# Kernel optimization log

Hardware: AMD Instinct MI355X
Metric: run time of the kernel (lower is better)

## Reference

```python
import jax, jax.numpy as jnp
import numpy as np

B, NELEC, D, NION = 2048, 32, 512, 8
NSPIN = 2
N = NELEC // NSPIN  # electrons per spin = orbital-matrix size = 16


def setup_inputs() -> dict:
    key = jax.random.key(0)
    ks = jax.random.split(key, 6)
    eq_inputs = jax.random.normal(ks[0], (B, NELEC, D), jnp.float32)
    r_ei = jax.random.normal(ks[1], (B, NELEC, NION, 3), jnp.float32)
    # learned params (stacked over the 2 spins; equal split so shapes match)
    W_lin = jax.random.normal(ks[2], (NSPIN, 2 * D, N), jnp.float32) * (0.5 / np.sqrt(D))
    b_lin = jax.random.normal(ks[3], (NSPIN, N), jnp.float32) * 0.1
    A_env = jax.random.normal(ks[4], (NSPIN, 3, 3, NION, N), jnp.float32) * 0.3
    w_ion = jax.random.normal(ks[5], (NSPIN, NION, N), jnp.float32)
    return dict(eq_inputs=eq_inputs, r_ei=r_ei, W_lin=W_lin, b_lin=b_lin,
                A_env=A_env, w_ion=w_ion)


def reference(eq_inputs, r_ei, W_lin, b_lin, A_env, w_ion):
    """Per-particle determinant antiequivariance layer.

    For each spin s and particle p, a doubly-equivariant orbital matrix
    M_p[j, k] = (y_p . W1[:,k] + y_j . W2[:,k] + b[k]) * env[j, k]
    is built (pair-concat dense split into two einsums to avoid the (B,n,n,2d)
    intermediate), with anisotropic exponential envelopes
    env[j, k] = sum_I w_ion[I,k] * exp(-||A[:,:,I,k] @ r_ei[j,I,:]||).
    Output per spin: y_p * det(M_p), stacked over spins -> (B, 2, n, d).
    """
    b, nelec, d = eq_inputs.shape
    n = nelec // NSPIN
    x = eq_inputs.reshape(b, NSPIN, n, d)            # spin_split=2 equal split
    r = r_ei.reshape(b, NSPIN, n, r_ei.shape[-2], 3)
    W1, W2 = W_lin[:, :d], W_lin[:, d:]
    # linear (doubly equivariant) part: (B, S, n_p, n_j, n_k)
    lin_p = jnp.einsum('bspf,sfk->bspk', x, W1)
    lin_j = jnp.einsum('bsjf,sfk->bsjk', x, W2) + b_lin[None, :, None, :]
    lin = lin_p[:, :, :, None, :] + lin_j[:, :, None, :, :]
    # anisotropic exponential envelopes: exp(-||A (r - R)||), combined over ions
    ar = jnp.einsum('bsjip,spqik->bsjiqk', r, A_env)        # (B,S,n,I,3,k)
    env = jnp.exp(-jnp.sqrt(jnp.sum(ar * ar, axis=-2)))     # (B,S,n,I,k)
    env = jnp.einsum('bsjik,sik->bsjk', env, w_ion)         # (B,S,n_j,n_k)
    M = lin * env[:, :, None, :, :]                         # (B,S,n_p,n_j,n_k)
    dets = jnp.linalg.det(M)                                # (B,S,n_p)
    # y_p * det(M_p), per spin (stacked over the spin axis)
    return x * dets[..., None]                              # (B,S,n,d)
```

## Files before the change

kernel.cpp:

```cpp
#include <hip/hip_runtime.h>
#include <cstdint>
#include <cstddef>

#define NSPIN 2
#define NPART 16
#define DDIM  512
#define NION  8
#define NB    2

#define RS_OFF     0
#define GRAM_OFF   768
#define LINP_OFF   (GRAM_OFF + 1152)
#define LINJ_OFF   (LINP_OFF + 320)
#define ENV_OFF    (LINJ_OFF + 320)
#define DETS_OFF   (ENV_OFF + 320)
#define LDS_FLOATS (DETS_OFF + 16)
#define LDS_BYTES  (LDS_FLOATS * 4)

#define WS_GRAM_F  16384

typedef short bf16x8 __attribute__((ext_vector_type(8)));
typedef float f32x4  __attribute__((ext_vector_type(4)));

__device__ __forceinline__ short bfc(float x) {
    unsigned u = __float_as_uint(x);
    u += 0x7FFFu + ((u >> 16) & 1u);
    return (short)(u >> 16);
}

#define DPPMAXU(k, ctrl) { unsigned o_ = (unsigned)__builtin_amdgcn_update_dpp(0, (int)(k), (ctrl), 0xF, 0xF, true); (k) = (k) > o_ ? (k) : o_; }

__global__ void __launch_bounds__(256)
prep_kernel(const float* __restrict__ WL, const float* __restrict__ AE,
            const float* __restrict__ WI, float* __restrict__ WSF)
{
    const int t = threadIdx.x;
    if (blockIdx.x < 16) {
        int slot = blockIdx.x * 256 + t;
        int spin = slot >> 11;
        int rem  = slot & 2047;
        int half = rem >> 10;
        int ks   = (rem >> 6) & 15;
        int lane = rem & 63;
        int cc2  = lane & 15, hh = lane >> 4;
        const float* src = WL + (size_t)spin * (2 * DDIM * NPART)
                         + ((size_t)(half * 512 + ks * 32 + hh * 8)) * NPART + cc2;
        ushort u[8];
        #pragma unroll
        for (int e = 0; e < 8; ++e) u[e] = (ushort)bfc(src[e * NPART]);
        uint4 pk;
        pk.x = (unsigned)u[0] | ((unsigned)u[1] << 16);
        pk.y = (unsigned)u[2] | ((unsigned)u[3] << 16);
        pk.z = (unsigned)u[4] | ((unsigned)u[5] << 16);
        pk.w = (unsigned)u[6] | ((unsigned)u[7] << 16);
        ((uint4*)WSF)[slot] = pk;
    } else {
        int s  = t >> 7;
        int ke = (t >> 3) & 15;
        int i  = t & 7;
        const float* Ag = AE + (size_t)s * (9 * NION * NPART);
        float a00 = Ag[((0 * 3 + 0) * NION + i) * NPART + ke];
        float a01 = Ag[((0 * 3 + 1) * NION + i) * NPART + ke];
        float a02 = Ag[((0 * 3 + 2) * NION + i) * NPART + ke];
        float a10 = Ag[((1 * 3 + 0) * NION + i) * NPART + ke];
        float a11 = Ag[((1 * 3 + 1) * NION + i) * NPART + ke];
        float a12 = Ag[((1 * 3 + 2) * NION + i) * NPART + ke];
        float a20 = Ag[((2 * 3 + 0) * NION + i) * NPART + ke];
        float a21 = Ag[((2 * 3 + 1) * NION + i) * NPART + ke];
        float a22 = Ag[((2 * 3 + 2) * NION + i) * NPART + ke];
        float* g = WSF + WS_GRAM_F + t * 8;
        g[0] = a00 * a00 + a01 * a01 + a02 * a02;
        g[1] = a10 * a10 + a11 * a11 + a12 * a12;
        g[2] = a20 * a20 + a21 * a21 + a22 * a22;
        g[3] = a00 * a10 + a01 * a11 + a02 * a12;
        g[4] = a00 * a20 + a01 * a21 + a02 * a22;
        g[5] = a10 * a20 + a11 * a21 + a12 * a22;
        g[6] = WI[(size_t)s * (NION * NPART) + i * NPART + ke];
        g[7] = 0.f;
    }
}

__global__ void __launch_bounds__(128, 4)
ppdet_kernel(const float* __restrict__ EQ, const float* __restrict__ RE,
             const float* __restrict__ WSF, const float* __restrict__ BL,
             float* __restrict__ OUT)
{
    extern __shared__ float ls[];
    const int t  = threadIdx.x;
    const int s  = blockIdx.x >> 10;
    const int b0 = (blockIdx.x & 1023) * NB;

    const int l  = t & 63;
    const int w  = t >> 6;
    const int c  = l & 15;
    const int h4 = l >> 4;
    const int jr = t & 15;

    #pragma unroll
    for (int it = 0; it < 6; ++it) {
        int idx = it * 128 + t;
        int ibuf = idx / 384, rem = idx % 384;
        int e = rem >> 4, j = rem & 15;
        ls[RS_OFF + idx] = RE[((size_t)(b0 + ibuf) * 32 + s * 16 + j) * 24 + e];
    }
    #pragma unroll
    for (int it = 0; it < 8; ++it) {
        int idx = it * 128 + t;
        int ke = idx >> 6, rem = idx & 63;
        ls[GRAM_OFF + ke * 72 + rem] = WSF[WS_GRAM_F + s * 1024 + idx];
    }
    const float blv = BL[s * NPART + c];
    __syncthreads();

    for (int ib = 0; ib < NB; ++ib) {
        const int b = b0 + ib;

        {
            const float* xg = EQ + ((size_t)(b * 32 + s * 16 + c)) * DDIM + h4 * 8;
            const uint4* wb = (const uint4*)WSF + (size_t)s * 2048 + w * 1024;
            f32x4 acc = {0.f, 0.f, 0.f, 0.f};
            #pragma unroll
            for (int kb = 0; kb < 4; ++kb) {
                float4 xa[8];
                uint4 wv[4];
                #pragma unroll
                for (int u = 0; u < 4; ++u) {
                    xa[2 * u]     = *(const float4*)(xg + (kb * 4 + u) * 32);
                    xa[2 * u + 1] = *(const float4*)(xg + (kb * 4 + u) * 32 + 4);
                    wv[u] = wb[(kb * 4 + u) * 64 + l];
                }
                #pragma unroll
                for (int u = 0; u < 4; ++u) {
                    bf16x8 af;
                    af[0] = bfc(xa[2 * u].x);     af[1] = bfc(xa[2 * u].y);
                    af[2] = bfc(xa[2 * u].z);     af[3] = bfc(xa[2 * u].w);
                    af[4] = bfc(xa[2 * u + 1].x); af[5] = bfc(xa[2 * u + 1].y);
                    af[6] = bfc(xa[2 * u + 1].z); af[7] = bfc(xa[2 * u + 1].w);
                    acc = __builtin_amdgcn_mfma_f32_16x16x32_bf16(af, *(bf16x8*)&wv[u], acc, 0, 0, 0);
                }
            }
            if (w == 0) {
                #pragma unroll
                for (int q = 0; q < 4; ++q)
                    ls[LINP_OFF + (h4 * 4 + q) * 20 + c] = acc[q];
            } else {
                #pragma unroll
                for (int q = 0; q < 4; ++q)
                    ls[LINJ_OFF + (h4 * 4 + q) * 20 + c] = acc[q] + blv;
            }
        }

        {
            const int ke8 = t >> 4;
            #pragma unroll
            for (int kx = 0; kx < 2; ++kx) {
                const int ke2 = (ke8 + kx * 8) & 15;
                const float4* gp = (const float4*)(ls + GRAM_OFF + ke2 * 72);
                float ev = 0.f;
                #pragma unroll
                for (int i = 0; i < 8; ++i) {
                    float4 gA = gp[i * 2];
                    float4 gB = gp[i * 2 + 1];
                    float r0 = ls[RS_OFF + ib * 384 + (i * 3 + 0) * 16 + jr];
                    float r1 = ls[RS_OFF + ib * 384 + (i * 3 + 1) * 16 + jr];
                    float r2 = ls[RS_OFF + ib * 384 + (i * 3 + 2) * 16 + jr];
                    float ss = r0 * r0 * gA.x;
                    ss = fmaf(r1 * r1, gA.y, ss);
                    ss = fmaf(r2 * r2, gA.z, ss);
                    float tcr = r0 * r1 * gA.w;
                    tcr = fmaf(r0 * r2, gB.x, tcr);
                    tcr = fmaf(r1 * r2, gB.y, tcr);
                    ss = fmaf(2.f, tcr, ss);
                    ss = fmaxf(ss, 0.f);
                    ev = fmaf(gB.z, __expf(-__builtin_amdgcn_sqrtf(ss)), ev);
                }
                ls[ENV_OFF + jr * 20 + ke2] = ev;
            }
        }
        __syncthreads();

        {
            const int lanebase4 = (t & 48) << 2;
            #pragma unroll
            for (int half = 0; half < 2; ++half) {
                const int p = (t >> 4) + half * 8;
                float Mr[16];
                const float* lp = ls + LINP_OFF + p * 20;
                const float* lj = ls + LINJ_OFF + jr * 20;
                const float* ev = ls + ENV_OFF  + jr * 20;
                #pragma unroll
                for (int cq = 0; cq < 4; ++cq) {
                    float4 a  = *(const float4*)(lp + cq * 4);
                    float4 bb = *(const float4*)(lj + cq * 4);
                    float4 e  = *(const float4*)(ev + cq * 4);
                    Mr[cq * 4 + 0] = (a.x + bb.x) * e.x;
                    Mr[cq * 4 + 1] = (a.y + bb.y) * e.y;
                    Mr[cq * 4 + 2] = (a.z + bb.z) * e.z;
                    Mr[cq * 4 + 3] = (a.w + bb.w) * e.w;
                }
                float detv = 1.f;
                unsigned sel = 0u;
                int inv = 0;
                bool msel = false;
                #pragma unroll
                for (int cc = 0; cc < 16; ++cc) {
                    unsigned key = msel ? 0u
                        : ((__float_as_uint(fabsf(Mr[cc])) & 0xFFFFFFF0u) | (unsigned)jr);
                    DPPMAXU(key, 0x121); DPPMAXU(key, 0x122); DPPMAXU(key, 0x124); DPPMAXU(key, 0x128);
                    const int idx = (int)(key & 15u);
                    const bool ispiv = (jr == idx) && !msel;
                    const int srcaddr = lanebase4 | (idx << 2);
                    float Pr[16];
                    #pragma unroll
                    for (int k2 = cc; k2 < 16; ++k2)
                        Pr[k2] = __int_as_float(__builtin_amdgcn_ds_bpermute(
                                     srcaddr, __float_as_int(Mr[k2])));
                    const float pv = Pr[cc];
                    const float f = (msel || ispiv || pv == 0.f) ? 0.f
                                  : Mr[cc] * __builtin_amdgcn_rcpf(pv);
                    inv += __popc(sel >> (idx + 1));
                    sel |= (1u << idx);
                    msel = msel || ispiv;
                    detv *= pv;
                    #pragma unroll
                    for (int k2 = cc + 1; k2 < 16; ++k2)
                        Mr[k2] = fmaf(-f, Pr[k2], Mr[k2]);
                }
                if (inv & 1) detv = -detv;
                if (jr == 0) ls[DETS_OFF + p] = detv;
            }
        }
        __syncthreads();

        {
            const size_t base = ((size_t)(b * 32 + s * 16)) * DDIM;
            #pragma unroll
            for (int i2 = 0; i2 < 16; ++i2) {
                int f4i = i2 * 128 + t;
                float dt = ls[DETS_OFF + i2];
                float4 xv = ((const float4*)(EQ + base))[f4i];
                ((float4*)(OUT + base))[f4i] =
                    make_float4(xv.x * dt, xv.y * dt, xv.z * dt, xv.w * dt);
            }
        }
    }
}

extern "C" void kernel_launch(void* const* d_in, const int* in_sizes, int n_in,
                              void* d_out, int out_size, void* d_ws, size_t ws_size,
                              hipStream_t stream) {
    const float* EQ = (const float*)d_in[0];
    const float* RE = (const float*)d_in[1];
    const float* WL = (const float*)d_in[2];
    const float* BL = (const float*)d_in[3];
    const float* AE = (const float*)d_in[4];
    const float* WI = (const float*)d_in[5];
    float* OUT = (float*)d_out;
    float* WSF = (float*)d_ws;
    (void)in_sizes; (void)n_in; (void)out_size; (void)ws_size;

    prep_kernel<<<dim3(17), dim3(256), 0, stream>>>(WL, AE, WI, WSF);
    ppdet_kernel<<<dim3(2048), dim3(128), LDS_BYTES, stream>>>(EQ, RE, WSF, BL, OUT);
}
```

Baseline: 87.99 us.

## Process four batches per 256-thread block with fused dual-GEMM waves

Each block now handles four batch elements with 256 threads. Each wave computes both lin_p and lin_j MFMA accumulations for one batch, with double-buffered x loads. The envelope and determinant phases are batched across the four elements with fewer barriers, and bf16 conversion uses the packed intrinsic. The goal is better amortisation of per-block setup and latency hiding, at the cost of more LDS per block and more register pressure.

```diff
diff --git a/kernel.cpp b/kernel.cpp
--- a/kernel.cpp
+++ b/kernel.cpp
@@ -1,4 +1,5 @@
 #include <hip/hip_runtime.h>
+#include <hip/hip_bf16.h>
 #include <cstdint>
 #include <cstddef>
 
@@ -6,15 +7,15 @@
 #define NPART 16
 #define DDIM  512
 #define NION  8
-#define NB    2
+#define NB    4
 
 #define RS_OFF     0
-#define GRAM_OFF   768
+#define GRAM_OFF   1536
 #define LINP_OFF   (GRAM_OFF + 1152)
-#define LINJ_OFF   (LINP_OFF + 320)
-#define ENV_OFF    (LINJ_OFF + 320)
-#define DETS_OFF   (ENV_OFF + 320)
-#define LDS_FLOATS (DETS_OFF + 16)
+#define LINJ_OFF   (LINP_OFF + 1280)
+#define ENV_OFF    (LINJ_OFF + 1280)
+#define DETS_OFF   (ENV_OFF + 1280)
+#define LDS_FLOATS (DETS_OFF + 64)
 #define LDS_BYTES  (LDS_FLOATS * 4)
 
 #define WS_GRAM_F  16384
@@ -26,6 +27,17 @@
     unsigned u = __float_as_uint(x);
     u += 0x7FFFu + ((u >> 16) & 1u);
     return (short)(u >> 16);
+}
+
+union AFU { bf16x8 v; __hip_bfloat162 h[4]; };
+
+__device__ __forceinline__ bf16x8 cvt8(const float4& a, const float4& b) {
+    AFU u;
+    u.h[0] = __float22bfloat162_rn(make_float2(a.x, a.y));
+    u.h[1] = __float22bfloat162_rn(make_float2(a.z, a.w));
+    u.h[2] = __float22bfloat162_rn(make_float2(b.x, b.y));
+    u.h[3] = __float22bfloat162_rn(make_float2(b.z, b.w));
+    return u.v;
 }
 
 #define DPPMAXU(k, ctrl) { unsigned o_ = (unsigned)__builtin_amdgcn_update_dpp(0, (int)(k), (ctrl), 0xF, 0xF, true); (k) = (k) > o_ ? (k) : o_; }
@@ -80,168 +92,170 @@
     }
 }
 
-__global__ void __launch_bounds__(128, 4)
+__global__ void __launch_bounds__(256, 4)
 ppdet_kernel(const float* __restrict__ EQ, const float* __restrict__ RE,
              const float* __restrict__ WSF, const float* __restrict__ BL,
              float* __restrict__ OUT)
 {
     extern __shared__ float ls[];
     const int t  = threadIdx.x;
-    const int s  = blockIdx.x >> 10;
-    const int b0 = (blockIdx.x & 1023) * NB;
+    const int s  = blockIdx.x >> 9;
+    const int b0 = (blockIdx.x & 511) * NB;
 
     const int l  = t & 63;
     const int w  = t >> 6;
     const int c  = l & 15;
     const int h4 = l >> 4;
     const int jr = t & 15;
+    const int ke = t >> 4;
 
     #pragma unroll
     for (int it = 0; it < 6; ++it) {
-        int idx = it * 128 + t;
+        int idx = it * 256 + t;
         int ibuf = idx / 384, rem = idx % 384;
         int e = rem >> 4, j = rem & 15;
         ls[RS_OFF + idx] = RE[((size_t)(b0 + ibuf) * 32 + s * 16 + j) * 24 + e];
     }
     #pragma unroll
-    for (int it = 0; it < 8; ++it) {
-        int idx = it * 128 + t;
-        int ke = idx >> 6, rem = idx & 63;
-        ls[GRAM_OFF + ke * 72 + rem] = WSF[WS_GRAM_F + s * 1024 + idx];
-    }
-    const float blv = BL[s * NPART + c];
-    __syncthreads();
-
-    for (int ib = 0; ib < NB; ++ib) {
-        const int b = b0 + ib;
-
-        {
-            const float* xg = EQ + ((size_t)(b * 32 + s * 16 + c)) * DDIM + h4 * 8;
-            const uint4* wb = (const uint4*)WSF + (size_t)s * 2048 + w * 1024;
-            f32x4 acc = {0.f, 0.f, 0.f, 0.f};
-            #pragma unroll
-            for (int kb = 0; kb < 4; ++kb) {
-                float4 xa[8];
-                uint4 wv[4];
+    for (int it = 0; it < 4; ++it) {
+        int idx = it * 256 + t;
+        int kk = idx >> 6, rem = idx & 63;
+        ls[GRAM_OFF + kk * 72 + rem] = WSF[WS_GRAM_F + s * 1024 + idx];
+    }
+
+    {
+        const float* xg  = EQ + ((size_t)((b0 + w) * 32 + s * 16 + c)) * DDIM + h4 * 8;
+        const uint4* wb1 = (const uint4*)WSF + (size_t)s * 2048;
+        const uint4* wb2 = wb1 + 1024;
+        f32x4 accp = {0.f, 0.f, 0.f, 0.f}, accj = {0.f, 0.f, 0.f, 0.f};
+        float4 xA[8], xB[8];
+        #pragma unroll
+        for (int u = 0; u < 4; ++u) {
+            xA[2 * u]     = *(const float4*)(xg + u * 32);
+            xA[2 * u + 1] = *(const float4*)(xg + u * 32 + 4);
+        }
+        #pragma unroll
+        for (int kb = 0; kb < 4; ++kb) {
+            float4* cur = (kb & 1) ? xB : xA;
+            float4* nxt = (kb & 1) ? xA : xB;
+            if (kb < 3) {
                 #pragma unroll
                 for (int u = 0; u < 4; ++u) {
-                    xa[2 * u]     = *(const float4*)(xg + (kb * 4 + u) * 32);
-                    xa[2 * u + 1] = *(const float4*)(xg + (kb * 4 + u) * 32 + 4);
-                    wv[u] = wb[(kb * 4 + u) * 64 + l];
+                    nxt[2 * u]     = *(const float4*)(xg + (kb + 1) * 128 + u * 32);
+                    nxt[2 * u + 1] = *(const float4*)(xg + (kb + 1) * 128 + u * 32 + 4);
                 }
-                #pragma unroll
-                for (int u = 0; u < 4; ++u) {
-                    bf16x8 af;
-                    af[0] = bfc(xa[2 * u].x);     af[1] = bfc(xa[2 * u].y);
-                    af[2] = bfc(xa[2 * u].z);     af[3] = bfc(xa[2 * u].w);
-                    af[4] = bfc(xa[2 * u + 1].x); af[5] = bfc(xa[2 * u + 1].y);
-                    af[6] = bfc(xa[2 * u + 1].z); af[7] = bfc(xa[2 * u + 1].w);
-                    acc = __builtin_amdgcn_mfma_f32_16x16x32_bf16(af, *(bf16x8*)&wv[u], acc, 0, 0, 0);
-                }
-            }
-            if (w == 0) {
-                #pragma unroll
-                for (int q = 0; q < 4; ++q)
-                    ls[LINP_OFF + (h4 * 4 + q) * 20 + c] = acc[q];
-            } else {
-                #pragma unroll
-                for (int q = 0; q < 4; ++q)
-                    ls[LINJ_OFF + (h4 * 4 + q) * 20 + c] = acc[q] + blv;
-            }
-        }
-
-        {
-            const int ke8 = t >> 4;
-            #pragma unroll
-            for (int kx = 0; kx < 2; ++kx) {
-                const int ke2 = (ke8 + kx * 8) & 15;
-                const float4* gp = (const float4*)(ls + GRAM_OFF + ke2 * 72);
-                float ev = 0.f;
-                #pragma unroll
-                for (int i = 0; i < 8; ++i) {
-                    float4 gA = gp[i * 2];
-                    float4 gB = gp[i * 2 + 1];
-                    float r0 = ls[RS_OFF + ib * 384 + (i * 3 + 0) * 16 + jr];
-                    float r1 = ls[RS_OFF + ib * 384 + (i * 3 + 1) * 16 + jr];
-                    float r2 = ls[RS_OFF + ib * 384 + (i * 3 + 2) * 16 + jr];
-                    float ss = r0 * r0 * gA.x;
-                    ss = fmaf(r1 * r1, gA.y, ss);
-                    ss = fmaf(r2 * r2, gA.z, ss);
-                    float tcr = r0 * r1 * gA.w;
-                    tcr = fmaf(r0 * r2, gB.x, tcr);
-                    tcr = fmaf(r1 * r2, gB.y, tcr);
-                    ss = fmaf(2.f, tcr, ss);
-                    ss = fmaxf(ss, 0.f);
-                    ev = fmaf(gB.z, __expf(-__builtin_amdgcn_sqrtf(ss)), ev);
-                }
-                ls[ENV_OFF + jr * 20 + ke2] = ev;
-            }
-        }
-        __syncthreads();
-
-        {
-            const int lanebase4 = (t & 48) << 2;
-            #pragma unroll
-            for (int half = 0; half < 2; ++half) {
-                const int p = (t >> 4) + half * 8;
-                float Mr[16];
-                const float* lp = ls + LINP_OFF + p * 20;
-                const float* lj = ls + LINJ_OFF + jr * 20;
-                const float* ev = ls + ENV_OFF  + jr * 20;
-                #pragma unroll
-                for (int cq = 0; cq < 4; ++cq) {
-                    float4 a  = *(const float4*)(lp + cq * 4);
-                    float4 bb = *(const float4*)(lj + cq * 4);
-                    float4 e  = *(const float4*)(ev + cq * 4);
-                    Mr[cq * 4 + 0] = (a.x + bb.x) * e.x;
-                    Mr[cq * 4 + 1] = (a.y + bb.y) * e.y;
-                    Mr[cq * 4 + 2] = (a.z + bb.z) * e.z;
-                    Mr[cq * 4 + 3] = (a.w + bb.w) * e.w;
-                }
-                float detv = 1.f;
-                unsigned sel = 0u;
-                int inv = 0;
-                bool msel = false;
-                #pragma unroll
-                for (int cc = 0; cc < 16; ++cc) {
-                    unsigned key = msel ? 0u
-                        : ((__float_as_uint(fabsf(Mr[cc])) & 0xFFFFFFF0u) | (unsigned)jr);
-                    DPPMAXU(key, 0x121); DPPMAXU(key, 0x122); DPPMAXU(key, 0x124); DPPMAXU(key, 0x128);
-                    const int idx = (int)(key & 15u);
-                    const bool ispiv = (jr == idx) && !msel;
-                    const int srcaddr = lanebase4 | (idx << 2);
-                    float Pr[16];
-                    #pragma unroll
-                    for (int k2 = cc; k2 < 16; ++k2)
-                        Pr[k2] = __int_as_float(__builtin_amdgcn_ds_bpermute(
-                                     srcaddr, __float_as_int(Mr[k2])));
-                    const float pv = Pr[cc];
-                    const float f = (msel || ispiv || pv == 0.f) ? 0.f
-                                  : Mr[cc] * __builtin_amdgcn_rcpf(pv);
-                    inv += __popc(sel >> (idx + 1));
-                    sel |= (1u << idx);
-                    msel = msel || ispiv;
-                    detv *= pv;
-                    #pragma unroll
-                    for (int k2 = cc + 1; k2 < 16; ++k2)
-                        Mr[k2] = fmaf(-f, Pr[k2], Mr[k2]);
-                }
-                if (inv & 1) detv = -detv;
-                if (jr == 0) ls[DETS_OFF + p] = detv;
-            }
-        }
-        __syncthreads();
-
-        {
-            const size_t base = ((size_t)(b * 32 + s * 16)) * DDIM;
-            #pragma unroll
-            for (int i2 = 0; i2 < 16; ++i2) {
-                int f4i = i2 * 128 + t;
-                float dt = ls[DETS_OFF + i2];
-                float4 xv = ((const float4*)(EQ + base))[f4i];
-                ((float4*)(OUT + base))[f4i] =
-                    make_float4(xv.x * dt, xv.y * dt, xv.z * dt, xv.w * dt);
-            }
+            }
+            uint4 w1v[4], w2v[4];
+            #pragma unroll
+            for (int u = 0; u < 4; ++u) {
+                w1v[u] = wb1[(kb * 4 + u) * 64 + l];
+                w2v[u] = wb2[(kb * 4 + u) * 64 + l];
+            }
+            #pragma unroll
+            for (int u = 0; u < 4; ++u) {
+                bf16x8 af = cvt8(cur[2 * u], cur[2 * u + 1]);
+                accp = __builtin_amdgcn_mfma_f32_16x16x32_bf16(af, *(bf16x8*)&w1v[u], accp, 0, 0, 0);
+                accj = __builtin_amdgcn_mfma_f32_16x16x32_bf16(af, *(bf16x8*)&w2v[u], accj, 0, 0, 0);
+            }
+        }
+        const float blv = BL[s * NPART + c];
+        #pragma unroll
+        for (int q = 0; q < 4; ++q) {
+            ls[LINP_OFF + (w * 16 + h4 * 4 + q) * 20 + c] = accp[q];
+            ls[LINJ_OFF + (w * 16 + h4 * 4 + q) * 20 + c] = accj[q] + blv;
+        }
+    }
+    __syncthreads();
+
+    {
+        const float4* gp = (const float4*)(ls + GRAM_OFF + ke * 72);
+        float ev[NB] = {0.f, 0.f, 0.f, 0.f};
+        #pragma unroll
+        for (int i = 0; i < 8; ++i) {
+            float4 gA = gp[2 * i];
+            float4 gB = gp[2 * i + 1];
+            #pragma unroll
+            for (int ib = 0; ib < NB; ++ib) {
+                const float* rs = ls + RS_OFF + ib * 384;
+                float r0 = rs[(i * 3 + 0) * 16 + jr];
+                float r1 = rs[(i * 3 + 1) * 16 + jr];
+                float r2 = rs[(i * 3 + 2) * 16 + jr];
+                float ss = r0 * r0 * gA.x;
+                ss = fmaf(r1 * r1, gA.y, ss);
+                ss = fmaf(r2 * r2, gA.z, ss);
+                float tcr = r0 * r1 * gA.w;
+                tcr = fmaf(r0 * r2, gB.x, tcr);
+                tcr = fmaf(r1 * r2, gB.y, tcr);
+                ss = fmaf(2.f, tcr, ss);
+                ss = fmaxf(ss, 0.f);
+                ev[ib] = fmaf(gB.z, __expf(-__builtin_amdgcn_sqrtf(ss)), ev[ib]);
+            }
+        }
+        #pragma unroll
+        for (int ib = 0; ib < NB; ++ib)
+            ls[ENV_OFF + (ib * 16 + jr) * 20 + ke] = ev[ib];
+    }
+    __syncthreads();
+
+    const int lanebase4 = (t & 48) << 2;
+    for (int ib = 0; ib < NB; ++ib) {
+        float Mr[16];
+        const float* lp = ls + LINP_OFF + (ib * 16 + ke) * 20;
+        const float* lj = ls + LINJ_OFF + (ib * 16 + jr) * 20;
+        const float* ev = ls + ENV_OFF  + (ib * 16 + jr) * 20;
+        #pragma unroll
+        for (int cq = 0; cq < 4; ++cq) {
+            float4 a  = *(const float4*)(lp + cq * 4);
+            float4 bb = *(const float4*)(lj + cq * 4);
+            float4 e  = *(const float4*)(ev + cq * 4);
+            Mr[cq * 4 + 0] = (a.x + bb.x) * e.x;
+            Mr[cq * 4 + 1] = (a.y + bb.y) * e.y;
+            Mr[cq * 4 + 2] = (a.z + bb.z) * e.z;
+            Mr[cq * 4 + 3] = (a.w + bb.w) * e.w;
+        }
+        float detv = 1.f;
+        unsigned sel = 0u;
+        int inv = 0;
+        bool msel = false;
+        #pragma unroll
+        for (int cc = 0; cc < 16; ++cc) {
+            unsigned key = msel ? 0u
+                : ((__float_as_uint(fabsf(Mr[cc])) & 0xFFFFFFF0u) | (unsigned)jr);
+            DPPMAXU(key, 0x121); DPPMAXU(key, 0x122); DPPMAXU(key, 0x124); DPPMAXU(key, 0x128);
+            const int idx = (int)(key & 15u);
+            const bool ispiv = (jr == idx) && !msel;
+            const int srcaddr = lanebase4 | (idx << 2);
+            float Pr[16];
+            #pragma unroll
+            for (int k2 = cc; k2 < 16; ++k2)
+                Pr[k2] = __int_as_float(__builtin_amdgcn_ds_bpermute(
+                             srcaddr, __float_as_int(Mr[k2])));
+            const float pv = Pr[cc];
+            const float f = (msel || ispiv || pv == 0.f) ? 0.f
+                          : Mr[cc] * __builtin_amdgcn_rcpf(pv);
+            inv += __popc(sel >> (idx + 1));
+            sel |= (1u << idx);
+            msel = msel || ispiv;
+            detv *= pv;
+            #pragma unroll
+            for (int k2 = cc + 1; k2 < 16; ++k2)
+                Mr[k2] = fmaf(-f, Pr[k2], Mr[k2]);
+        }
+        if (inv & 1) detv = -detv;
+        if (jr == 0) ls[DETS_OFF + ib * 16 + ke] = detv;
+    }
+    __syncthreads();
+
+    #pragma unroll
+    for (int ib = 0; ib < NB; ++ib) {
+        const size_t base = ((size_t)((b0 + ib) * 32 + s * 16)) * DDIM;
+        #pragma unroll
+        for (int i2 = 0; i2 < 8; ++i2) {
+            int f4i = i2 * 256 + t;
+            float dt = ls[DETS_OFF + ib * 16 + (f4i >> 7)];
+            float4 xv = ((const float4*)(EQ + base))[f4i];
+            ((float4*)(OUT + base))[f4i] =
+                make_float4(xv.x * dt, xv.y * dt, xv.z * dt, xv.w * dt);
         }
     }
 }
@@ -260,5 +274,5 @@
     (void)in_sizes; (void)n_in; (void)out_size; (void)ws_size;
 
     prep_kernel<<<dim3(17), dim3(256), 0, stream>>>(WL, AE, WI, WSF);
-    ppdet_kernel<<<dim3(2048), dim3(128), LDS_BYTES, stream>>>(EQ, RE, WSF, BL, OUT);
-}
+    ppdet_kernel<<<dim3(1024), dim3(256), LDS_BYTES, stream>>>(EQ, RE, WSF, BL, OUT);
+}
```

New measurement: 82.24 us. -6.5%, faster.
